# Kernel optimization log

Hardware: AMD Instinct MI355X
Metric: run time of the kernel (lower is better)

## Reference

```python
import jax, jax.numpy as jnp
import numpy as np

B, L, D = 2, 2048, 768
H = 12
HD = D // H  # 64
SCALE = HD ** -0.5


def setup_inputs() -> dict:
    key = jax.random.key(0)
    k1, k2, k3 = jax.random.split(key, 3)
    x = jax.random.normal(k1, (B, L, D), dtype=jnp.float32)
    mask = jnp.ones((B, L), dtype=jnp.int32)
    # nn.Linear weights: [out_features, in_features]
    Wqkv = jax.random.normal(k2, (3 * D, D), dtype=jnp.float32) * (D ** -0.5)
    bqkv = jnp.zeros((3 * D,), dtype=jnp.float32)
    Wout = jax.random.normal(k3, (D, D), dtype=jnp.float32) * (D ** -0.5)
    bout = jnp.zeros((D,), dtype=jnp.float32)
    return {"x": x, "mask": mask, "Wqkv": Wqkv, "bqkv": bqkv, "Wout": Wout, "bout": bout}


def reference(x, mask, Wqkv, bqkv, Wout, bout):
    Bx, Lx, Dx = x.shape
    # qkv projection: [B,L,3D] -> [3,B,H,L,HD]
    qkv = x @ Wqkv.T + bqkv
    qkv = qkv.reshape(Bx, Lx, 3, H, HD).transpose(2, 0, 3, 1, 4)
    q, k, v = qkv[0], qkv[1], qkv[2]
    # scores [B,H,L,L]
    attn = jnp.einsum('bhqd,bhkd->bhqk', q, k) * SCALE
    attn = jnp.where(mask[:, None, None, :] == 0, -jnp.inf, attn)
    attn = jax.nn.softmax(attn, axis=-1)
    # dropout p=0.0 -> identity
    out = jnp.einsum('bhqk,bhkd->bhqd', attn, v)
    out = out.transpose(0, 2, 1, 3).reshape(Bx, Lx, Dx)
    return out @ Wout.T + bout
```

## Files before the change

### kernel.cpp

```cpp
#include <hip/hip_runtime.h>
#include <hip/hip_bf16.h>

#define DEV __device__ __forceinline__

typedef __bf16 bf16_t;
typedef bf16_t bf16x8 __attribute__((ext_vector_type(8)));
typedef float f32x4 __attribute__((ext_vector_type(4)));
typedef float f32x16 __attribute__((ext_vector_type(16)));
typedef unsigned int u32x4 __attribute__((ext_vector_type(4)));

constexpr int Bc = 2, Lc = 2048, Dc = 768, Hc = 12, HDc = 64;
constexpr int NTOK = Bc * Lc;
constexpr int QKVN = 3 * Dc;
constexpr float ATT_SCALE = 0.125f;
constexpr float LOG2E = 1.44269504088896f;

DEV unsigned short f2bf(float f) {
  unsigned int u = __builtin_bit_cast(unsigned int, f);
  u += 0x7FFFu + ((u >> 16) & 1u);
  return (unsigned short)(u >> 16);
}

DEV bf16x8 ld16(const unsigned short* p) {
  return __builtin_bit_cast(bf16x8, *reinterpret_cast<const u32x4*>(p));
}

DEV unsigned cvtpk(float lo, float hi) {
  unsigned r;
  asm("v_cvt_pk_bf16_f32 %0, %1, %2" : "=v"(r) : "v"(lo), "v"(hi));
  return r;
}

DEV void gload16(const unsigned short* g, unsigned short* l) {
  __builtin_amdgcn_global_load_lds(
      (const __attribute__((address_space(1))) unsigned int*)g,
      (__attribute__((address_space(3))) unsigned int*)l, 16, 0, 0);
}

__global__ __launch_bounds__(256) void prep_kernel(
    const float* __restrict__ x, const float* __restrict__ Wqkv,
    const float* __restrict__ Wout, const int* __restrict__ mask,
    unsigned short* __restrict__ xb, unsigned short* __restrict__ wqkvb,
    unsigned short* __restrict__ woutb, float* __restrict__ mb,
    int* __restrict__ mflag) {
  const int bid = blockIdx.x, tid = threadIdx.x;
  const float* src; unsigned short* dst; int base;
  if (bid < 3072)      { src = x;    dst = xb;    base = bid; }
  else if (bid < 4800) { src = Wqkv; dst = wqkvb; base = bid - 3072; }
  else if (bid < 5376) { src = Wout; dst = woutb; base = bid - 4800; }
  else {
    int i = (bid - 5376) * 256 + tid;
    int mv = mask[i];
    mb[i] = mv ? 0.f : -1e30f;
    unsigned long long anyz = __ballot(mv == 0);
    if ((tid & 63) == 0) mflag[i >> 6] = (anyz != 0ull) ? 1 : 0;
    return;
  }
  int i = (base * 256 + tid) * 4;
  float4 v = *reinterpret_cast<const float4*>(src + i);
  ushort4 o;
  o.x = f2bf(v.x); o.y = f2bf(v.y); o.z = f2bf(v.z); o.w = f2bf(v.w);
  *reinterpret_cast<ushort4*>(dst + i) = o;
}

template <int MODE>
__global__ __launch_bounds__(256) void gemm_bt(
    const unsigned short* __restrict__ A,
    const unsigned short* __restrict__ Bw,
    const float* __restrict__ bias,
    unsigned short* __restrict__ qb, unsigned short* __restrict__ kb,
    unsigned short* __restrict__ vtb,
    float* __restrict__ Y,
    int M, int N, int K) {
  constexpr int BM = 128, BN = 128, BK = 64;
  __shared__ alignas(16) unsigned short a_lds[BM * BK];
  __shared__ alignas(16) unsigned short b_lds[BN * BK];
  __shared__ alignas(16) unsigned short qk_patch[(MODE == 0) ? 4 : 1][16][72];

  const int tid = threadIdx.x;
  const int lane = tid & 63;
  const int l15 = lane & 15, lg = lane >> 4;
  const int wave = tid >> 6;
  const int wr = wave >> 1, wc = wave & 1;

  const int ntiles = N / BN;
  const int m0 = (blockIdx.x / ntiles) * BM;
  const int n0 = (blockIdx.x % ntiles) * BN;

  f32x4 acc[4][4] = {};

  for (int k0 = 0; k0 < K; k0 += BK) {
#pragma unroll
    for (int i = 0; i < 4; ++i) {
      int cc = i * 256 + tid;
      int row = cc >> 3, col = (cc & 7) * 8;
      gload16(A + (size_t)(m0 + row) * K + k0 + col, &a_lds[(i * 256 + wave * 64) * 8]);
      gload16(Bw + (size_t)(n0 + row) * K + k0 + col, &b_lds[(i * 256 + wave * 64) * 8]);
    }
    __syncthreads();
#pragma unroll
    for (int kk = 0; kk < 2; ++kk) {
      bf16x8 af[4], bfr[4];
#pragma unroll
      for (int m = 0; m < 4; ++m) {
        int row = wr * 64 + m * 16 + l15;
        af[m] = ld16(&a_lds[row * BK + kk * 32 + lg * 8]);
      }
#pragma unroll
      for (int n = 0; n < 4; ++n) {
        int row = wc * 64 + n * 16 + l15;
        bfr[n] = ld16(&b_lds[row * BK + kk * 32 + lg * 8]);
      }
#pragma unroll
      for (int m = 0; m < 4; ++m)
#pragma unroll
        for (int n = 0; n < 4; ++n)
          acc[m][n] = __builtin_amdgcn_mfma_f32_16x16x32_bf16(af[m], bfr[n], acc[m][n], 0, 0, 0);
    }
    __syncthreads();
  }

  if constexpr (MODE == 0) {
    const int base_col = n0 + wc * 64;
    const int s = base_col / Dc;
    const int h = (base_col % Dc) >> 6;
    if (s == 2) {
#pragma unroll
      for (int m = 0; m < 4; ++m) {
        int lq = m0 + wr * 64 + m * 16 + lg * 4;
        int b = lq >> 11, lql = lq & 2047;
#pragma unroll
        for (int n = 0; n < 4; ++n) {
          int d = n * 16 + l15;
          float bv = bias[base_col + n * 16 + l15];
          ushort4 o;
#pragma unroll
          for (int j = 0; j < 4; ++j)
            ((unsigned short*)&o)[j] = f2bf(acc[m][n][j] + bv);
          *reinterpret_cast<ushort4*>(
              vtb + ((size_t)(b * Hc + h) * HDc + d) * Lc + lql) = o;
        }
      }
    } else {
      unsigned short* dst = (s == 0) ? qb : kb;
      const float sc = (s == 0) ? (ATT_SCALE * LOG2E) : 1.0f;
#pragma unroll
      for (int m = 0; m < 4; ++m) {
#pragma unroll
        for (int n = 0; n < 4; ++n) {
          float bv = bias[base_col + n * 16 + l15];
#pragma unroll
          for (int j = 0; j < 4; ++j)
            qk_patch[wave][lg * 4 + j][n * 16 + l15] =
                f2bf((acc[m][n][j] + bv) * sc);
        }
#pragma unroll
        for (int i = 0; i < 2; ++i) {
          int task = i * 64 + lane;
          int r = task >> 3, ch = task & 7;
          int lq = m0 + wr * 64 + m * 16 + r;
          int b = lq >> 11, lql = lq & 2047;
          u32x4 v = *reinterpret_cast<const u32x4*>(&qk_patch[wave][r][ch * 8]);
          *reinterpret_cast<u32x4*>(
              dst + ((size_t)(b * Hc + h) * Lc + lql) * HDc + ch * 8) = v;
        }
      }
    }
  } else {
#pragma unroll
    for (int m = 0; m < 4; ++m) {
      int row_base = m0 + wr * 64 + m * 16 + lg * 4;
#pragma unroll
      for (int n = 0; n < 4; ++n) {
        int col = n0 + wc * 64 + n * 16 + l15;
        float bv = bias[col];
#pragma unroll
        for (int j = 0; j < 4; ++j)
          Y[(size_t)(row_base + j) * Dc + col] = acc[m][n][j] + bv;
      }
    }
  }
}

__global__ __launch_bounds__(256) void attn_kernel(
    const unsigned short* __restrict__ qb,
    const unsigned short* __restrict__ kb,
    const unsigned short* __restrict__ vtb,
    const float* __restrict__ mb,
    const int* __restrict__ mflag,
    unsigned short* __restrict__ aout) {
  __shared__ alignas(16) unsigned short k_lds[4][4096];
  __shared__ alignas(16) unsigned short v_lds[2][4096];
  __shared__ float l_lds[2][32];
  const int tid = threadIdx.x;
  const int lane = tid & 63;
  const int l31 = lane & 31;
  const int hi = lane >> 5;
  const int wave = tid >> 6;
  const int ws = wave & 1;
  const int g = wave >> 1;
  const int f = blockIdx.x;
  const int loc = f >> 3;
  const int bh = (f & 7) * 3 + (loc >> 5);
  const int b = bh / Hc, h = bh % Hc;
  const int q0 = (loc & 31) * 64 + ws * 32;

  const unsigned short* Kbh = kb + (size_t)bh * Lc * HDc;
  const unsigned short* Vbh = vtb + (size_t)bh * HDc * Lc;
  const float* mbb = mb + b * Lc + hi * 4;
  const int* mfp = mflag + b * (Lc / 64);

  unsigned long long mbits;
  {
    int mv = (lane < 32) ? mfp[lane] : 0;
    mbits = __ballot(mv != 0);
  }

  bf16x8 qf[4];
  {
    const unsigned short* Qp = qb + ((size_t)bh * Lc + q0 + l31) * HDc + hi * 8;
#pragma unroll
    for (int c = 0; c < 4; ++c) qf[c] = ld16(Qp + c * 16);
  }

  bf16x8 onesf;
  {
    u32x4 ow = {0x3F803F80u, 0x3F803F80u, 0x3F803F80u, 0x3F803F80u};
    onesf = __builtin_bit_cast(bf16x8, ow);
  }

  f32x16 accO[2] = {};
  f32x16 accL = {};

  const int j0 = wave * 2, j1 = j0 + 1;
  const int r80 = j0 * 8 + (lane >> 3), r81 = r80 + 8;
  const int csw0 = (((lane & 7) ^ (lane >> 3) ^ (j0 & 3))) << 3;
  const int csw1 = (((lane & 7) ^ (lane >> 3) ^ (j1 & 3))) << 3;
  const unsigned short* kp0 = Kbh + (size_t)r80 * HDc + csw0;
  const unsigned short* kp1 = Kbh + (size_t)r81 * HDc + csw1;
  const unsigned short* vp0 = Vbh + (size_t)r80 * Lc + csw0;
  const unsigned short* vp1 = Vbh + (size_t)r81 * Lc + csw1;

#define STAGEK(buf)                               \
  {                                               \
    gload16(kp0, &k_lds[buf][j0 * 512]);          \
    gload16(kp1, &k_lds[buf][j1 * 512]);          \
    kp0 += 64 * HDc; kp1 += 64 * HDc;             \
  }
#define STAGEV(buf)                               \
  {                                               \
    gload16(vp0, &v_lds[buf][j0 * 512]);          \
    gload16(vp1, &v_lds[buf][j1 * 512]);          \
    vp0 += 64; vp1 += 64;                         \
  }

  const int swz = ((l31 & 7) ^ (l31 >> 3)) << 3;
  const int krow = (g * 32 + l31) * 64;

  STAGEK(0) STAGEK(1) STAGEV(0)
  asm volatile("s_waitcnt vmcnt(0)" ::: "memory");
  __builtin_amdgcn_s_barrier();
  f32x16 s = {};
#pragma unroll
  for (int c = 0; c < 4; ++c) {
    int ch = (((c * 2 + hi) << 3) ^ swz);
    s = __builtin_amdgcn_mfma_f32_32x32x16_bf16(
        ld16(&k_lds[0][0] + krow + ch), qf[c], s, 0, 0, 0);
  }
  STAGEK(2) STAGEV(1)

  constexpr int NSTEP = Lc / 64;
  for (int t = 0; t < NSTEP; ++t) {
    if (t + 3 < NSTEP) STAGEK((t + 3) & 3)

    f32x16 s2 = {};
    if (t + 1 < NSTEP) {
      const unsigned short* kl = &k_lds[(t + 1) & 3][0];
      __builtin_amdgcn_s_setprio(1);
#pragma unroll
      for (int c = 0; c < 4; ++c) {
        int ch = (((c * 2 + hi) << 3) ^ swz);
        s2 = __builtin_amdgcn_mfma_f32_32x32x16_bf16(
            ld16(kl + krow + ch), qf[c], s2, 0, 0, 0);
      }
      __builtin_amdgcn_s_setprio(0);
    }

    if ((mbits >> t) & 1ull) {
      const int kvt = t * 64 + g * 32;
#pragma unroll
      for (int gg = 0; gg < 4; ++gg) {
        float4 m0v = *reinterpret_cast<const float4*>(mbb + kvt + gg * 8);
        s[gg * 4 + 0] += m0v.x; s[gg * 4 + 1] += m0v.y;
        s[gg * 4 + 2] += m0v.z; s[gg * 4 + 3] += m0v.w;
      }
    }
#pragma unroll
    for (int i = 0; i < 16; ++i) s[i] = __builtin_amdgcn_exp2f(s[i]);
    bf16x8 pf[2];
#pragma unroll
    for (int c = 0; c < 2; ++c) {
      const int o = c * 8;
      unsigned pk01 = cvtpk(s[o + 0], s[o + 1]);
      unsigned pk23 = cvtpk(s[o + 2], s[o + 3]);
      unsigned pk45 = cvtpk(s[o + 4], s[o + 5]);
      unsigned pk67 = cvtpk(s[o + 6], s[o + 7]);
      asm("v_permlane32_swap_b32 %0, %1" : "+v"(pk01), "+v"(pk45));
      asm("v_permlane32_swap_b32 %0, %1" : "+v"(pk23), "+v"(pk67));
      u32x4 w = {pk01, pk23, pk45, pk67};
      pf[c] = __builtin_bit_cast(bf16x8, w);
    }
    accL = __builtin_amdgcn_mfma_f32_32x32x16_bf16(onesf, pf[0], accL, 0, 0, 0);
    accL = __builtin_amdgcn_mfma_f32_32x32x16_bf16(onesf, pf[1], accL, 0, 0, 0);
    {
      const unsigned short* vl = &v_lds[t & 1][0];
      __builtin_amdgcn_s_setprio(1);
#pragma unroll
      for (int dt = 0; dt < 2; ++dt) {
#pragma unroll
        for (int c = 0; c < 2; ++c) {
          int ch = (((g * 4 + c * 2 + hi) << 3) ^ swz);
          accO[dt] = __builtin_amdgcn_mfma_f32_32x32x16_bf16(
              ld16(vl + (dt * 32 + l31) * 64 + ch), pf[c], accO[dt], 0, 0, 0);
        }
      }
      __builtin_amdgcn_s_setprio(0);
    }
    if (t < NSTEP - 3) {
      asm volatile("s_waitcnt vmcnt(2)" ::: "memory");
    } else {
      asm volatile("s_waitcnt vmcnt(0)" ::: "memory");
    }
    __builtin_amdgcn_s_barrier();
    __builtin_amdgcn_sched_barrier(0);
    if (t + 2 < NSTEP) STAGEV((t) & 1)
    s = s2;
  }

  __syncthreads();
  const float l_run = accL[0];
  float* mO = (float*)&k_lds[0][0];
  if (g == 1) {
#pragma unroll
    for (int dt = 0; dt < 2; ++dt)
#pragma unroll
      for (int i = 0; i < 16; ++i)
        mO[(ws * 32 + dt * 16 + i) * 64 + lane] = accO[dt][i];
    if (hi == 0) l_lds[ws][l31] = l_run;
  }
  __syncthreads();
  if (g == 0) {
    float rl = 1.0f / (l_run + l_lds[ws][l31]);
    const int q = q0 + l31;
    unsigned short* op = aout + ((size_t)(b * Lc + q)) * Dc + h * HDc;
#pragma unroll
    for (int dt = 0; dt < 2; ++dt)
#pragma unroll
      for (int gg = 0; gg < 4; ++gg) {
        ushort4 o;
#pragma unroll
        for (int j = 0; j < 4; ++j) {
          int i = gg * 4 + j;
          float v = (accO[dt][i] + mO[(ws * 32 + dt * 16 + i) * 64 + lane]) * rl;
          ((unsigned short*)&o)[j] = f2bf(v);
        }
        *reinterpret_cast<ushort4*>(op + dt * 32 + gg * 8 + hi * 4) = o;
      }
  }
}

extern "C" void kernel_launch(void* const* d_in, const int* in_sizes, int n_in,
                              void* d_out, int out_size, void* d_ws, size_t ws_size,
                              hipStream_t stream) {
  const float* x    = (const float*)d_in[0];
  const int*   mask = (const int*)d_in[1];
  const float* Wqkv = (const float*)d_in[2];
  const float* bqkv = (const float*)d_in[3];
  const float* Wout = (const float*)d_in[4];
  const float* bout = (const float*)d_in[5];
  float* out = (float*)d_out;

  constexpr size_t NX   = (size_t)NTOK * Dc;
  constexpr size_t NWQ  = (size_t)QKVN * Dc;
  constexpr size_t NWO  = (size_t)Dc * Dc;
  unsigned short* w = (unsigned short*)d_ws;
  unsigned short* xb    = w;            w += NX;
  unsigned short* wqkvb = w;            w += NWQ;
  unsigned short* woutb = w;            w += NWO;
  unsigned short* qbuf  = w;            w += NX;
  unsigned short* kbuf  = w;            w += NX;
  unsigned short* vtb   = w;            w += NX;
  unsigned short* aoutb = w;            w += NX;
  float* mbf = (float*)w;               w += 2 * NTOK;
  int* mflag = (int*)w;

  prep_kernel<<<5392, 256, 0, stream>>>(x, Wqkv, Wout, mask, xb, wqkvb, woutb, mbf, mflag);

  gemm_bt<0><<<(NTOK / 128) * (QKVN / 128), 256, 0, stream>>>(
      xb, wqkvb, bqkv, qbuf, kbuf, vtb, nullptr, NTOK, QKVN, Dc);

  attn_kernel<<<dim3(768), 256, 0, stream>>>(qbuf, kbuf, vtb, mbf, mflag, aoutb);

  gemm_bt<1><<<(NTOK / 128) * (Dc / 128), 256, 0, stream>>>(
      aoutb, woutb, bout, nullptr, nullptr, nullptr, out, NTOK, Dc, Dc);
}
```

Measured before the change: 113.0 us.

## Retile projection GEMMs to 96-wide N tiles and swizzle block order

```diff
diff --git a/kernel.cpp b/kernel.cpp
--- a/kernel.cpp
+++ b/kernel.cpp
@@ -72,10 +72,13 @@
     unsigned short* __restrict__ vtb,
     float* __restrict__ Y,
     int M, int N, int K) {
-  constexpr int BM = 128, BN = 128, BK = 64;
+  constexpr int BM = (MODE == 0) ? 128 : 64;
+  constexpr int BN = 96, BK = 64;
+  constexpr int AI = BM * BK / 2048;
+  constexpr int MR = BM / 32;
   __shared__ alignas(16) unsigned short a_lds[BM * BK];
   __shared__ alignas(16) unsigned short b_lds[BN * BK];
-  __shared__ alignas(16) unsigned short qk_patch[(MODE == 0) ? 4 : 1][16][72];
+  __shared__ alignas(16) unsigned short qk_patch[(MODE == 0) ? 4 : 1][16][56];
 
   const int tid = threadIdx.x;
   const int lane = tid & 63;
@@ -83,56 +86,64 @@
   const int wave = tid >> 6;
   const int wr = wave >> 1, wc = wave & 1;
 
-  const int ntiles = N / BN;
-  const int m0 = (blockIdx.x / ntiles) * BM;
-  const int n0 = (blockIdx.x % ntiles) * BN;
-
-  f32x4 acc[4][4] = {};
+  const int nm = M / BM;
+  const int nwg = nm * (N / BN);
+  const int t = (blockIdx.x & 7) * (nwg >> 3) + (blockIdx.x >> 3);
+  const int m0 = (t % nm) * BM;
+  const int n0 = (t / nm) * BN;
+
+  f32x4 acc[MR][3] = {};
 
   for (int k0 = 0; k0 < K; k0 += BK) {
 #pragma unroll
-    for (int i = 0; i < 4; ++i) {
+    for (int i = 0; i < AI; ++i) {
       int cc = i * 256 + tid;
       int row = cc >> 3, col = (cc & 7) * 8;
       gload16(A + (size_t)(m0 + row) * K + k0 + col, &a_lds[(i * 256 + wave * 64) * 8]);
+    }
+#pragma unroll
+    for (int i = 0; i < 3; ++i) {
+      int cc = i * 256 + tid;
+      int row = cc >> 3, col = (cc & 7) * 8;
       gload16(Bw + (size_t)(n0 + row) * K + k0 + col, &b_lds[(i * 256 + wave * 64) * 8]);
     }
     __syncthreads();
 #pragma unroll
     for (int kk = 0; kk < 2; ++kk) {
-      bf16x8 af[4], bfr[4];
-#pragma unroll
-      for (int m = 0; m < 4; ++m) {
-        int row = wr * 64 + m * 16 + l15;
+      bf16x8 af[MR], bfr[3];
+#pragma unroll
+      for (int m = 0; m < MR; ++m) {
+        int row = wr * (MR * 16) + m * 16 + l15;
         af[m] = ld16(&a_lds[row * BK + kk * 32 + lg * 8]);
       }
 #pragma unroll
-      for (int n = 0; n < 4; ++n) {
-        int row = wc * 64 + n * 16 + l15;
+      for (int n = 0; n < 3; ++n) {
+        int row = wc * 48 + n * 16 + l15;
         bfr[n] = ld16(&b_lds[row * BK + kk * 32 + lg * 8]);
       }
 #pragma unroll
-      for (int m = 0; m < 4; ++m)
-#pragma unroll
-        for (int n = 0; n < 4; ++n)
+      for (int m = 0; m < MR; ++m)
+#pragma unroll
+        for (int n = 0; n < 3; ++n)
           acc[m][n] = __builtin_amdgcn_mfma_f32_16x16x32_bf16(af[m], bfr[n], acc[m][n], 0, 0, 0);
     }
     __syncthreads();
   }
 
   if constexpr (MODE == 0) {
-    const int base_col = n0 + wc * 64;
-    const int s = base_col / Dc;
-    const int h = (base_col % Dc) >> 6;
+    const int base_col = n0 + wc * 48;
+    const int s = n0 / Dc;
     if (s == 2) {
 #pragma unroll
       for (int m = 0; m < 4; ++m) {
         int lq = m0 + wr * 64 + m * 16 + lg * 4;
         int b = lq >> 11, lql = lq & 2047;
 #pragma unroll
-        for (int n = 0; n < 4; ++n) {
-          int d = n * 16 + l15;
-          float bv = bias[base_col + n * 16 + l15];
+        for (int n = 0; n < 3; ++n) {
+          int cbase = base_col + n * 16;
+          int h = (cbase % Dc) >> 6;
+          int d = (cbase & 63) + l15;
+          float bv = bias[cbase + l15];
           ushort4 o;
 #pragma unroll
           for (int j = 0; j < 4; ++j)
@@ -147,7 +158,7 @@
 #pragma unroll
       for (int m = 0; m < 4; ++m) {
 #pragma unroll
-        for (int n = 0; n < 4; ++n) {
+        for (int n = 0; n < 3; ++n) {
           float bv = bias[base_col + n * 16 + l15];
 #pragma unroll
           for (int j = 0; j < 4; ++j)
@@ -157,22 +168,27 @@
 #pragma unroll
         for (int i = 0; i < 2; ++i) {
           int task = i * 64 + lane;
-          int r = task >> 3, ch = task & 7;
-          int lq = m0 + wr * 64 + m * 16 + r;
-          int b = lq >> 11, lql = lq & 2047;
-          u32x4 v = *reinterpret_cast<const u32x4*>(&qk_patch[wave][r][ch * 8]);
-          *reinterpret_cast<u32x4*>(
-              dst + ((size_t)(b * Hc + h) * Lc + lql) * HDc + ch * 8) = v;
+          if (task < 96) {
+            int r = task / 6, ch = task - r * 6;
+            int gcol = base_col + ch * 8;
+            int h = (gcol % Dc) >> 6;
+            int d0 = gcol & 63;
+            int lq = m0 + wr * 64 + m * 16 + r;
+            int b = lq >> 11, lql = lq & 2047;
+            u32x4 v = *reinterpret_cast<const u32x4*>(&qk_patch[wave][r][ch * 8]);
+            *reinterpret_cast<u32x4*>(
+                dst + ((size_t)(b * Hc + h) * Lc + lql) * HDc + d0) = v;
+          }
         }
       }
     }
   } else {
 #pragma unroll
-    for (int m = 0; m < 4; ++m) {
-      int row_base = m0 + wr * 64 + m * 16 + lg * 4;
-#pragma unroll
-      for (int n = 0; n < 4; ++n) {
-        int col = n0 + wc * 64 + n * 16 + l15;
+    for (int m = 0; m < MR; ++m) {
+      int row_base = m0 + wr * (MR * 16) + m * 16 + lg * 4;
+#pragma unroll
+      for (int n = 0; n < 3; ++n) {
+        int col = n0 + wc * 48 + n * 16 + l15;
         float bv = bias[col];
 #pragma unroll
         for (int j = 0; j < 4; ++j)
@@ -396,11 +412,11 @@
 
   prep_kernel<<<5392, 256, 0, stream>>>(x, Wqkv, Wout, mask, xb, wqkvb, woutb, mbf, mflag);
 
-  gemm_bt<0><<<(NTOK / 128) * (QKVN / 128), 256, 0, stream>>>(
+  gemm_bt<0><<<(NTOK / 128) * (QKVN / 96), 256, 0, stream>>>(
       xb, wqkvb, bqkv, qbuf, kbuf, vtb, nullptr, NTOK, QKVN, Dc);
 
   attn_kernel<<<dim3(768), 256, 0, stream>>>(qbuf, kbuf, vtb, mbf, mflag, aoutb);
 
-  gemm_bt<1><<<(NTOK / 128) * (Dc / 128), 256, 0, stream>>>(
+  gemm_bt<1><<<(NTOK / 64) * (Dc / 96), 256, 0, stream>>>(
       aoutb, woutb, bout, nullptr, nullptr, nullptr, out, NTOK, Dc, Dc);
 }
```

Measured after the change: 93.13 us, median of 2. -17.5%, faster.
